# Kernel tuning notes

Hardware: AMD Instinct MI355X
Metric: run time of the kernel (lower is better)

The kernel has to match this reference:

```python
import jax, jax.numpy as jnp
import numpy as np

BSZ, SEQ, HID = 8, 4096, 1024
N_EXPERTS = 8
CAPACITY = 512  # expert_capacity_per_batch; effective cap = min(SEQ, CAPACITY)
SCALE = 1.0     # routed_scaling_factor


def setup_inputs() -> dict:
    key = jax.random.key(0)
    k1, k2 = jax.random.split(key)
    hidden_states = jax.random.normal(k1, (BSZ, SEQ, HID), dtype=jnp.float32)
    # kaiming_uniform_(a=sqrt(5)) on [d,e] -> bound = 1/sqrt(fan_in=d)
    bound = 1.0 / np.sqrt(HID)
    weight = jax.random.uniform(k2, (HID, N_EXPERTS), dtype=jnp.float32,
                                minval=-bound, maxval=bound)
    return {"hidden_states": hidden_states, "weight": weight}


def reference(hidden_states, weight):
    bsz, seq_len, h = hidden_states.shape
    # gating logits in fp32: [b, s, e]
    logits = jnp.einsum('bsd,de->bse', hidden_states.astype(jnp.float32),
                        weight.astype(jnp.float32))
    affinity = jax.nn.softmax(logits, axis=-1)          # [b, s, e]
    affinity = jnp.transpose(affinity, (0, 2, 1))       # [b, e, s]
    cap = min(seq_len, CAPACITY)                        # static
    # Each expert picks its top-`cap` tokens (sorted descending, like torch.topk)
    topk_scores, topk_indices = jax.lax.top_k(affinity, cap)  # [b, e, cap]
    topk_scores = topk_scores * SCALE
    # dense dispatch mask [b, e, cap, s]: one-hot over token positions
    dispatch_mask = jax.nn.one_hot(topk_indices, seq_len, dtype=jnp.float32)
    return topk_indices, topk_scores, dispatch_mask
```

## Files before the change

kernel.cpp:

```cpp
#include <hip/hip_runtime.h>

constexpr int BSZ = 8, SEQ = 4096, HID = 1024, NE = 8, CAP = 512;
constexpr int ROWS = BSZ * NE;
constexpr size_t IDX_ELEMS = (size_t)ROWS * CAP;
constexpr size_t SCR_OFF = IDX_ELEMS;
constexpr size_t MASK_OFF = IDX_ELEMS * 2;
constexpr size_t MASK_ELEMS = (size_t)ROWS * CAP * SEQ;
constexpr size_t AFF_ELEMS = (size_t)ROWS * SEQ;

__global__ __launch_bounds__(128) void gating_kernel(const float* __restrict__ hidden,
                                                     const float* __restrict__ weight,
                                                     float* __restrict__ aff)
{
    __shared__ float hls[16][68];
    __shared__ float wls[8][68];
    __shared__ float lls[16][8];

    const int tid = threadIdx.x;
    const int T0 = blockIdx.x * 16;
    const int t = tid >> 3;
    const int e = tid & 7;

    float v0 = 0.f, v1 = 0.f, v2 = 0.f, v3 = 0.f;
    for (int c = 0; c < 16; ++c) {
        __syncthreads();
#pragma unroll
        for (int k = 0; k < 2; ++k) {
            const int j = tid + k * 128;
            const int tt = j >> 4, q = j & 15;
            const float4 v = *(const float4*)(hidden + (size_t)(T0 + tt) * HID + c * 64 + 4 * q);
            *(float4*)&hls[tt][4 * q] = v;
        }
#pragma unroll
        for (int k = 0; k < 4; ++k) {
            const int j = tid + k * 128;
            const int dd = j >> 3, ee = j & 7;
            wls[ee][dd] = weight[(size_t)(c * 64 + dd) * NE + ee];
        }
        __syncthreads();
#pragma unroll
        for (int k = 0; k < 4; ++k) {
            const int base = 16 * k;
            const float4 hA = *(const float4*)&hls[t][base + 0];
            const float4 hB = *(const float4*)&hls[t][base + 4];
            const float4 hC = *(const float4*)&hls[t][base + 8];
            const float4 hD = *(const float4*)&hls[t][base + 12];
            const float4 wA = *(const float4*)&wls[e][base + 0];
            const float4 wB = *(const float4*)&wls[e][base + 4];
            const float4 wC = *(const float4*)&wls[e][base + 8];
            const float4 wD = *(const float4*)&wls[e][base + 12];
            v0 = __fadd_rn(__fmul_rn(hA.x, wA.x),
                 __fadd_rn(__fmul_rn(hB.x, wB.x),
                 __fadd_rn(__fmul_rn(hC.x, wC.x),
                 __fadd_rn(__fmul_rn(hD.x, wD.x), v0))));
            v1 = __fadd_rn(__fmul_rn(hA.y, wA.y),
                 __fadd_rn(__fmul_rn(hB.y, wB.y),
                 __fadd_rn(__fmul_rn(hC.y, wC.y),
                 __fadd_rn(__fmul_rn(hD.y, wD.y), v1))));
            v2 = __fadd_rn(__fmul_rn(hA.z, wA.z),
                 __fadd_rn(__fmul_rn(hB.z, wB.z),
                 __fadd_rn(__fmul_rn(hC.z, wC.z),
                 __fadd_rn(__fmul_rn(hD.z, wD.z), v2))));
            v3 = __fadd_rn(__fmul_rn(hA.w, wA.w),
                 __fadd_rn(__fmul_rn(hB.w, wB.w),
                 __fadd_rn(__fmul_rn(hC.w, wC.w),
                 __fadd_rn(__fmul_rn(hD.w, wD.w), v3))));
        }
    }
    const float logit = __fadd_rn(__fadd_rn(v0, v1), __fadd_rn(v2, v3));

    lls[t][e] = logit;
    __syncthreads();

    float l[8];
#pragma unroll
    for (int k = 0; k < 8; ++k) l[k] = lls[t][k];
    float m = l[0];
#pragma unroll
    for (int k = 1; k < 8; ++k) m = fmaxf(m, l[k]);
    float p[8];
#pragma unroll
    for (int k = 0; k < 8; ++k)
        p[k] = (float)exp((double)__fsub_rn(l[k], m));
    const float s = __fadd_rn(__fadd_rn(__fadd_rn(p[0], p[1]), __fadd_rn(p[2], p[3])),
                              __fadd_rn(__fadd_rn(p[4], p[5]), __fadd_rn(p[6], p[7])));
    const float a = __fdiv_rn(p[e], s);

    const int token = T0 + t;
    const int b = token >> 12;
    const int sidx = token & (SEQ - 1);
    aff[((size_t)b * NE + e) * SEQ + sidx] = a;
}

__global__ __launch_bounds__(1024) void topk_zero_kernel(const float* __restrict__ aff,
                                                         float* __restrict__ out,
                                                         long long zero_elems)
{
    __shared__ unsigned long long keys[SEQ];
    if (blockIdx.x < (unsigned)ROWS) {
        const int row = blockIdx.x;
        const float* a = aff + (size_t)row * SEQ;
        for (int i = threadIdx.x; i < SEQ; i += 1024) {
            const unsigned int fb = __float_as_uint(a[i]);
            keys[i] = ((unsigned long long)fb << 32) | (unsigned int)(SEQ - 1 - i);
        }
        for (int len = 2; len <= SEQ; len <<= 1) {
            for (int stride = len >> 1; stride > 0; stride >>= 1) {
                __syncthreads();
                for (int t = threadIdx.x; t < SEQ / 2; t += 1024) {
                    const int i = (t << 1) - (t & (stride - 1));
                    const int j = i + stride;
                    const unsigned long long ki = keys[i], kj = keys[j];
                    const bool desc = ((i & len) == 0);
                    if (desc ? (ki < kj) : (ki > kj)) { keys[i] = kj; keys[j] = ki; }
                }
            }
        }
        __syncthreads();
        if (threadIdx.x < CAP) {
            const int t = threadIdx.x;
            const unsigned long long k = keys[t];
            const int idx = (SEQ - 1) - (int)(unsigned int)(k & 0xffffffffu);
            out[(size_t)row * CAP + t] = (float)idx;
            out[SCR_OFF + (size_t)row * CAP + t] =
                __uint_as_float((unsigned int)(k >> 32));
        }
    } else {
        const long long nz4 = zero_elems >> 2;
        float4* mz = (float4*)(out + MASK_OFF);
        const float4 z4 = make_float4(0.f, 0.f, 0.f, 0.f);
        const long long stride = (long long)(gridDim.x - ROWS) * 1024;
        for (long long i = (long long)(blockIdx.x - ROWS) * 1024 + threadIdx.x;
             i < nz4; i += stride)
            mz[i] = z4;
    }
}

__global__ void tailzero_kernel(float* __restrict__ out)
{
    const long long n4 = (long long)(AFF_ELEMS >> 2);
    float4* mz = (float4*)(out + MASK_OFF + MASK_ELEMS - AFF_ELEMS);
    const long long i = (long long)blockIdx.x * blockDim.x + threadIdx.x;
    if (i < n4) mz[i] = make_float4(0.f, 0.f, 0.f, 0.f);
}

__global__ void scatter_kernel(float* __restrict__ out)
{
    const int p = blockIdx.x * blockDim.x + threadIdx.x;
    if (p < (int)IDX_ELEMS) {
        const int idx = (int)out[p];
        out[MASK_OFF + (size_t)p * SEQ + idx] = 1.0f;
    }
}

extern "C" void kernel_launch(void* const* d_in, const int* in_sizes, int n_in,
                              void* d_out, int out_size, void* d_ws, size_t ws_size,
                              hipStream_t stream)
{
    const float* hidden = (const float*)d_in[0];
    const float* weight = (const float*)d_in[1];
    float* out = (float*)d_out;

    const bool use_ws = (ws_size >= AFF_ELEMS * sizeof(float));
    float* aff = use_ws ? (float*)d_ws
                        : (out + MASK_OFF + MASK_ELEMS - AFF_ELEMS);

    gating_kernel<<<2048, 128, 0, stream>>>(hidden, weight, aff);

    const long long zero_elems = use_ws ? (long long)MASK_ELEMS
                                        : (long long)(MASK_ELEMS - AFF_ELEMS);
    topk_zero_kernel<<<ROWS + 1984, 1024, 0, stream>>>(aff, out, zero_elems);

    if (!use_ws)
        tailzero_kernel<<<256, 256, 0, stream>>>(out);

    scatter_kernel<<<(int)((IDX_ELEMS + 255) / 256), 256, 0, stream>>>(out);
}
```

Baseline: 650.0 us.

## Write dense dispatch mask in one pass instead of zero-fill plus scatter

The mask zero-fill is taken out of the top-k kernel, and the separate tail-zero and scatter kernels are removed. A new mask kernel writes every mask row directly with float4 stores, putting 1.0 where the position matches the selected index. This avoids a second pass of scattered writes over the mask and the extra kernel launches. In exchange, the top-k sort no longer overlaps with mask zeroing, so the sort now runs alone on only 64 blocks before the mask is written.

After: 680.5 us. +4.7%, slower.

```diff
diff --git a/kernel.cpp b/kernel.cpp
--- a/kernel.cpp
+++ b/kernel.cpp
@@ -92,64 +92,59 @@
     aff[((size_t)b * NE + e) * SEQ + sidx] = a;
 }
 
-__global__ __launch_bounds__(1024) void topk_zero_kernel(const float* __restrict__ aff,
-                                                         float* __restrict__ out,
-                                                         long long zero_elems)
+__global__ __launch_bounds__(1024) void topk_kernel(const float* __restrict__ aff,
+                                                    float* __restrict__ out)
 {
     __shared__ unsigned long long keys[SEQ];
-    if (blockIdx.x < (unsigned)ROWS) {
-        const int row = blockIdx.x;
-        const float* a = aff + (size_t)row * SEQ;
-        for (int i = threadIdx.x; i < SEQ; i += 1024) {
-            const unsigned int fb = __float_as_uint(a[i]);
-            keys[i] = ((unsigned long long)fb << 32) | (unsigned int)(SEQ - 1 - i);
-        }
-        for (int len = 2; len <= SEQ; len <<= 1) {
-            for (int stride = len >> 1; stride > 0; stride >>= 1) {
-                __syncthreads();
-                for (int t = threadIdx.x; t < SEQ / 2; t += 1024) {
-                    const int i = (t << 1) - (t & (stride - 1));
-                    const int j = i + stride;
-                    const unsigned long long ki = keys[i], kj = keys[j];
-                    const bool desc = ((i & len) == 0);
-                    if (desc ? (ki < kj) : (ki > kj)) { keys[i] = kj; keys[j] = ki; }
-                }
+    const int row = blockIdx.x;
+    const float* a = aff + (size_t)row * SEQ;
+    for (int i = threadIdx.x; i < SEQ; i += 1024) {
+        const unsigned int fb = __float_as_uint(a[i]);
+        keys[i] = ((unsigned long long)fb << 32) | (unsigned int)(SEQ - 1 - i);
+    }
+    for (int len = 2; len <= SEQ; len <<= 1) {
+        for (int stride = len >> 1; stride > 0; stride >>= 1) {
+            __syncthreads();
+            for (int t = threadIdx.x; t < SEQ / 2; t += 1024) {
+                const int i = (t << 1) - (t & (stride - 1));
+                const int j = i + stride;
+                const unsigned long long ki = keys[i], kj = keys[j];
+                const bool desc = ((i & len) == 0);
+                if (desc ? (ki < kj) : (ki > kj)) { keys[i] = kj; keys[j] = ki; }
             }
         }
-        __syncthreads();
-        if (threadIdx.x < CAP) {
-            const int t = threadIdx.x;
-            const unsigned long long k = keys[t];
-            const int idx = (SEQ - 1) - (int)(unsigned int)(k & 0xffffffffu);
-            out[(size_t)row * CAP + t] = (float)idx;
-            out[SCR_OFF + (size_t)row * CAP + t] =
-                __uint_as_float((unsigned int)(k >> 32));
-        }
-    } else {
-        const long long nz4 = zero_elems >> 2;
-        float4* mz = (float4*)(out + MASK_OFF);
-        const float4 z4 = make_float4(0.f, 0.f, 0.f, 0.f);
-        const long long stride = (long long)(gridDim.x - ROWS) * 1024;
-        for (long long i = (long long)(blockIdx.x - ROWS) * 1024 + threadIdx.x;
-             i < nz4; i += stride)
-            mz[i] = z4;
+    }
+    __syncthreads();
+    if (threadIdx.x < CAP) {
+        const int t = threadIdx.x;
+        const unsigned long long k = keys[t];
+        const int idx = (SEQ - 1) - (int)(unsigned int)(k & 0xffffffffu);
+        out[(size_t)row * CAP + t] = (float)idx;
+        out[SCR_OFF + (size_t)row * CAP + t] =
+            __uint_as_float((unsigned int)(k >> 32));
     }
 }
 
-__global__ void tailzero_kernel(float* __restrict__ out)
+__global__ __launch_bounds__(256) void mask_kernel(const float* __restrict__ idxf,
+                                                   float* __restrict__ mask)
 {
-    const long long n4 = (long long)(AFF_ELEMS >> 2);
-    float4* mz = (float4*)(out + MASK_OFF + MASK_ELEMS - AFF_ELEMS);
-    const long long i = (long long)blockIdx.x * blockDim.x + threadIdx.x;
-    if (i < n4) mz[i] = make_float4(0.f, 0.f, 0.f, 0.f);
-}
-
-__global__ void scatter_kernel(float* __restrict__ out)
-{
-    const int p = blockIdx.x * blockDim.x + threadIdx.x;
-    if (p < (int)IDX_ELEMS) {
-        const int idx = (int)out[p];
-        out[MASK_OFF + (size_t)p * SEQ + idx] = 1.0f;
+    const int t = threadIdx.x;
+    const int r0 = blockIdx.x * 4;
+#pragma unroll
+    for (int r = 0; r < 4; ++r) {
+        const int rc = r0 + r;
+        const int idx = (int)idxf[rc];
+        float* dst = mask + (size_t)rc * SEQ;
+#pragma unroll
+        for (int k = 0; k < 4; ++k) {
+            const int pos = (k * 256 + t) * 4;
+            float4 v;
+            v.x = (idx == pos + 0) ? 1.0f : 0.0f;
+            v.y = (idx == pos + 1) ? 1.0f : 0.0f;
+            v.z = (idx == pos + 2) ? 1.0f : 0.0f;
+            v.w = (idx == pos + 3) ? 1.0f : 0.0f;
+            *(float4*)(dst + pos) = v;
+        }
     }
 }
 
@@ -167,12 +162,7 @@
 
     gating_kernel<<<2048, 128, 0, stream>>>(hidden, weight, aff);
 
-    const long long zero_elems = use_ws ? (long long)MASK_ELEMS
-                                        : (long long)(MASK_ELEMS - AFF_ELEMS);
-    topk_zero_kernel<<<ROWS + 1984, 1024, 0, stream>>>(aff, out, zero_elems);
+    topk_kernel<<<ROWS, 1024, 0, stream>>>(aff, out);
 
-    if (!use_ws)
-        tailzero_kernel<<<256, 256, 0, stream>>>(out);
-
-    scatter_kernel<<<(int)((IDX_ELEMS + 255) / 256), 256, 0, stream>>>(out);
+    mask_kernel<<<(int)(IDX_ELEMS / 4), 256, 0, stream>>>(out, out + MASK_OFF);
 }
```
